# Kernel tuning notes

Hardware: AMD Instinct MI355X
Metric: run time of the kernel (lower is better)

Reference implementation:

```python
import jax, jax.numpy as jnp
import numpy as np

NUM_BINS = 16  # matches init kwarg num_bins


def setup_inputs() -> dict:
    key = jax.random.key(0)
    k1, k2, k3, k4, k5, k6, k7 = jax.random.split(key, 7)
    N, D, E, F = 100000, 256, 3200000, 4
    HID, NCLS = 256, 40
    x = jax.random.normal(k1, (N, D), dtype=jnp.float32)
    edge_index = jax.random.randint(k2, (E, 2), 0, N, dtype=jnp.int32)
    edge_features = jax.random.randint(k3, (E, F), 0, NUM_BINS, dtype=jnp.int32)
    # Dense layer params (keras Dense: y = x @ W + b)
    W1 = jax.random.normal(k4, (D, HID), dtype=jnp.float32) * 0.05
    b1 = jnp.zeros((HID,), dtype=jnp.float32)
    W2 = jax.random.normal(k5, (HID + F * NUM_BINS, NCLS), dtype=jnp.float32) * 0.05
    b2 = jnp.zeros((NCLS,), dtype=jnp.float32)
    return {"x": x, "edge_index": edge_index, "edge_features": edge_features,
            "W1": W1, "b1": b1, "W2": W2, "b2": b2}


def reference(x, edge_index, edge_features, W1, b1, W2, b2):
    N = x.shape[0]
    E, F = edge_features.shape

    h = jax.nn.relu(x @ W1 + b1)  # conv1: [N, HID]

    # per-feature one-hot + concat along axis 1 == reshape of [E,F,BINS]
    enc = jax.nn.one_hot(edge_features, NUM_BINS, dtype=h.dtype).reshape(E, F * NUM_BINS)

    seg = edge_index[:, 0]  # [E] node ids in [0, N)
    # Replicate tf.unique first-appearance indexing:
    #   segment_indices[j] = rank (by first appearance) of seg[j]
    #   mapped[e] = segment_indices[seg[e]] = rank[seg[seg[e]]]
    pos = jnp.full((N,), E, dtype=jnp.int32).at[seg].min(
        jnp.arange(E, dtype=jnp.int32))           # first edge position per node id
    rank = jnp.zeros((N,), jnp.int32).at[jnp.argsort(pos)].set(
        jnp.arange(N, dtype=jnp.int32))           # first-appearance rank per node id
    mapped = rank[jnp.take(seg, seg)]             # valid since N <= E

    # unsorted_segment_sum + zero padding to N rows == segment_sum with N segments
    agg = jax.ops.segment_sum(enc, mapped, num_segments=N)  # [N, F*BINS]

    z = jax.nn.relu(jnp.concatenate([h, agg], axis=1))
    return z @ W2 + b2  # conv2: [N, NCLS]
```

## Files before the change

### kernel.cpp

```cpp
#include <hip/hip_runtime.h>
#include <hip/hip_bf16.h>

#define WCHUNK 16
#define EPB  8192
#define TPB_MB 1024
#define BROWS 128
#define BCAP 16384

typedef __attribute__((ext_vector_type(8))) short bhalf8;
typedef __attribute__((ext_vector_type(4))) float floatx4;

__device__ __forceinline__ unsigned short f2bf(float f) {
    __hip_bfloat16 h = __float2bfloat16(f);
    union { __hip_bfloat16 h; unsigned short u; } v;
    v.h = h;
    return v.u;
}

__global__ void k_preps(const float* __restrict__ x, unsigned short* __restrict__ xbf,
                        const float* __restrict__ W1, const float* __restrict__ W2,
                        unsigned short* __restrict__ W1T, unsigned short* __restrict__ W2T,
                        int* __restrict__ pos, int* __restrict__ cursorb,
                        unsigned long long* __restrict__ bitmap,
                        int N, int total4, int nbuck, int W, int E, int nb_x, int nb_i) {
    int bid = blockIdx.x;
    int tid = threadIdx.x;
    if (bid < nb_x) {
        int f = bid * 256 + tid;
        if (f >= total4) return;
        int tile = f >> 12;
        int row = (f >> 6) & 63;
        int c4 = (f & 63) * 4;
        int grow = tile * 64 + row;
        float4 v = (grow < N) ? *reinterpret_cast<const float4*>(x + (size_t)grow * 256 + c4)
                              : make_float4(0.f, 0.f, 0.f, 0.f);
        ushort4 bv;
        bv.x = f2bf(v.x); bv.y = f2bf(v.y); bv.z = f2bf(v.z); bv.w = f2bf(v.w);
        int uidx = (row * 256 + c4) ^ ((row & 7) << 3);
        *reinterpret_cast<ushort4*>(&xbf[(size_t)tile * 16384 + uidx]) = bv;
    } else if (bid < nb_x + nb_i) {
        int i = (bid - nb_x) * 256 + tid;
        if (i < N) pos[i] = E;
        if (i < nbuck) cursorb[i] = i * BCAP;
        if (i < W) bitmap[i] = 0ull;
    } else {
        int i = (bid - nb_x - nb_i) * 256 + tid;
        if (i < 256 * 256) {
            int c = i >> 8, k = i & 255;
            W1T[i] = f2bf(W1[k * 256 + c]);
        }
        if (i < 48 * 320) {
            int c = i / 320, k = i % 320;
            W2T[i] = (c < 40) ? f2bf(W2[k * 40 + c]) : (unsigned short)0;
        }
    }
}

__global__ void k_posmin(const int* __restrict__ ei, int* __restrict__ pos, int Escan) {
    int e = blockIdx.x * blockDim.x + threadIdx.x;
    if (e < Escan) {
        int s = ((const int2*)ei)[e].x;
        if (pos[s] > e) atomicMin(&pos[s], e);
    }
}

__global__ void k_bitmap(const int* __restrict__ pos, unsigned long long* __restrict__ bitmap,
                         int N, int E) {
    int n = blockIdx.x * blockDim.x + threadIdx.x;
    if (n < N) {
        int p = pos[n];
        if (p < E) atomicOr(&bitmap[p >> 6], 1ull << (p & 63));
    }
}

__global__ void k_bitsum(const unsigned long long* __restrict__ bitmap,
                         int* __restrict__ bsum, int W) {
    __shared__ int sdata[256];
    int t = threadIdx.x;
    int base = (blockIdx.x * 256 + t) * WCHUNK;
    int cnt = 0;
    for (int l = 0; l < WCHUNK; l++) {
        int i = base + l;
        if (i < W) cnt += __popcll(bitmap[i]);
    }
    sdata[t] = cnt;
    __syncthreads();
    for (int s = 128; s > 0; s >>= 1) {
        if (t < s) sdata[t] += sdata[t + s];
        __syncthreads();
    }
    if (t == 0) bsum[blockIdx.x] = sdata[0];
}

__global__ void k_scanbsum(int* __restrict__ bsum, int nblk) {
    __shared__ int part[1024];
    const int T = 1024;
    int t = threadIdx.x;
    int per = (nblk + T - 1) / T;
    int s0 = t * per, s1 = min(s0 + per, nblk);
    int sum = 0;
    for (int i = s0; i < s1; i++) sum += bsum[i];
    part[t] = sum;
    __syncthreads();
    for (int off = 1; off < T; off <<= 1) {
        int v = 0;
        if (t >= off) v = part[t - off];
        __syncthreads();
        part[t] += v;
        __syncthreads();
    }
    int run = part[t] - sum;
    for (int i = s0; i < s1; i++) {
        int old = bsum[i];
        bsum[i] = run;
        run += old;
    }
    if (t == T - 1) bsum[nblk] = part[T - 1];
}

__global__ void k_wordpfx(const unsigned long long* __restrict__ bitmap,
                          const int* __restrict__ bsum, int* __restrict__ wordpfx, int W) {
    __shared__ int sdata[256];
    int t = threadIdx.x;
    int base = (blockIdx.x * 256 + t) * WCHUNK;
    int cnt = 0;
    for (int l = 0; l < WCHUNK; l++) {
        int i = base + l;
        if (i < W) cnt += __popcll(bitmap[i]);
    }
    sdata[t] = cnt;
    __syncthreads();
    for (int off = 1; off < 256; off <<= 1) {
        int v = 0;
        if (t >= off) v = sdata[t - off];
        __syncthreads();
        sdata[t] += v;
        __syncthreads();
    }
    int run = bsum[blockIdx.x] + sdata[t] - cnt;
    for (int l = 0; l < WCHUNK; l++) {
        int i = base + l;
        if (i >= W) break;
        wordpfx[i] = run;
        run += __popcll(bitmap[i]);
    }
}

__global__ void k_rt(const int* __restrict__ ei, const int* __restrict__ pos,
                     const unsigned long long* __restrict__ bitmap,
                     const int* __restrict__ wordpfx, int* __restrict__ rt, int N) {
    int n = blockIdx.x * blockDim.x + threadIdx.x;
    if (n >= N) return;
    int sn = ((const int2*)ei)[n].x;
    int p = pos[sn];
    int w = p >> 6, off = p & 63;
    unsigned long long mask = (1ull << off) - 1ull;
    rt[n] = wordpfx[w] + __popcll(bitmap[w] & mask);
}

__global__ __launch_bounds__(TPB_MB, 4) void k_mebin(const int* __restrict__ ei,
                                                     const int* __restrict__ rt,
                                                     const int* __restrict__ ef,
                                                     int* __restrict__ cursorb,
                                                     unsigned* __restrict__ binned,
                                                     int E, int nbuck) {
    __shared__ unsigned lmp[EPB];
    __shared__ int lcnt[800];
    __shared__ int lbase[800];
    __shared__ int lfill[800];
    int tid = threadIdx.x;
    int base = blockIdx.x * EPB;
    for (int b = tid; b < nbuck; b += TPB_MB) { lcnt[b] = 0; lfill[b] = 0; }
    __syncthreads();
#pragma unroll
    for (int jj = 0; jj < 2; jj++) {
        int l0 = (jj * 4 + 0) * TPB_MB + tid;
        int l1 = (jj * 4 + 1) * TPB_MB + tid;
        int l2 = (jj * 4 + 2) * TPB_MB + tid;
        int l3 = (jj * 4 + 3) * TPB_MB + tid;
        int e0 = base + l0, e1 = base + l1, e2 = base + l2, e3 = base + l3;
        int s0 = 0, s1 = 0, s2 = 0, s3 = 0;
        if (e0 < E) s0 = ((const int2*)ei)[e0].x;
        if (e1 < E) s1 = ((const int2*)ei)[e1].x;
        if (e2 < E) s2 = ((const int2*)ei)[e2].x;
        if (e3 < E) s3 = ((const int2*)ei)[e3].x;
        int m0 = 0, m1 = 0, m2 = 0, m3 = 0;
        if (e0 < E) m0 = rt[s0];
        if (e1 < E) m1 = rt[s1];
        if (e2 < E) m2 = rt[s2];
        if (e3 < E) m3 = rt[s3];
        int4 f0, f1, f2, f3;
        if (e0 < E) f0 = *reinterpret_cast<const int4*>(ef + 4 * (size_t)e0);
        if (e1 < E) f1 = *reinterpret_cast<const int4*>(ef + 4 * (size_t)e1);
        if (e2 < E) f2 = *reinterpret_cast<const int4*>(ef + 4 * (size_t)e2);
        if (e3 < E) f3 = *reinterpret_cast<const int4*>(ef + 4 * (size_t)e3);
        if (e0 < E) { lmp[l0] = ((unsigned)m0 << 16) | (unsigned)(f0.x | (f0.y << 4) | (f0.z << 8) | (f0.w << 12)); atomicAdd(&lcnt[m0 >> 7], 1); }
        if (e1 < E) { lmp[l1] = ((unsigned)m1 << 16) | (unsigned)(f1.x | (f1.y << 4) | (f1.z << 8) | (f1.w << 12)); atomicAdd(&lcnt[m1 >> 7], 1); }
        if (e2 < E) { lmp[l2] = ((unsigned)m2 << 16) | (unsigned)(f2.x | (f2.y << 4) | (f2.z << 8) | (f2.w << 12)); atomicAdd(&lcnt[m2 >> 7], 1); }
        if (e3 < E) { lmp[l3] = ((unsigned)m3 << 16) | (unsigned)(f3.x | (f3.y << 4) | (f3.z << 8) | (f3.w << 12)); atomicAdd(&lcnt[m3 >> 7], 1); }
    }
    __syncthreads();
    for (int b = tid; b < nbuck; b += TPB_MB) {
        int c = lcnt[b];
        lbase[b] = (c > 0) ? atomicAdd(&cursorb[b], c) : 0;
    }
    __syncthreads();
#pragma unroll
    for (int j = 0; j < EPB / TPB_MB; j++) {
        int li = j * TPB_MB + tid;
        if (base + li < E) {
            unsigned v = lmp[li];
            int b = v >> 23;
            int off = atomicAdd(&lfill[b], 1);
            long long slot = (long long)lbase[b] + off;
            if (slot < (long long)(b + 1) * BCAP)
                binned[slot] = v & 0x7FFFFFu;
        }
    }
}

__global__ __launch_bounds__(256) void k_bgather(const int* __restrict__ cursorb,
                                                 const unsigned* __restrict__ binned,
                                                 unsigned short* __restrict__ aggbf, int N) {
    __shared__ int hist[BROWS * 64];
    int tid = threadIdx.x;
    int b = blockIdx.x;
    int m0 = b * BROWS;
    for (int i = tid; i < BROWS * 64; i += 256) hist[i] = 0;
    __syncthreads();
    int r0 = b * BCAP;
    int r1 = min(cursorb[b], (b + 1) * BCAP);
    for (int i = r0 + tid; i < r1; i += 256) {
        unsigned v = binned[i];
        int lr = (int)(v >> 16) << 6;
        atomicAdd(&hist[lr + (v & 15u)], 1);
        atomicAdd(&hist[lr + 16 + ((v >> 4) & 15u)], 1);
        atomicAdd(&hist[lr + 32 + ((v >> 8) & 15u)], 1);
        atomicAdd(&hist[lr + 48 + ((v >> 12) & 15u)], 1);
    }
    __syncthreads();
    int rows = min(BROWS, N - m0);
    for (int i = tid; i < rows * 64; i += 256) {
        int lr = i >> 6, col = i & 63;
        int tile = (m0 + lr) >> 6;
        int row = (m0 + lr) & 63;
        int uidx = (row * 64 + col) ^ ((row & 7) << 3);
        aggbf[(size_t)tile * 4096 + uidx] = f2bf((float)hist[i]);
    }
}

__global__ __launch_bounds__(512) void k_fused(const unsigned short* __restrict__ xbf,
                                               const unsigned short* __restrict__ W1T,
                                               const float* __restrict__ b1,
                                               const unsigned short* __restrict__ W2T,
                                               const float* __restrict__ b2,
                                               const unsigned short* __restrict__ aggbf,
                                               float* __restrict__ out, int N) {
    __shared__ __align__(16) unsigned short xs[64 * 256];
    __shared__ __align__(16) unsigned short as[64 * 64];
    int tid = threadIdx.x;
    int lane = tid & 63;
    int w = tid >> 6;
    int lrow = lane & 15, lkb = lane >> 4;
    int n0 = blockIdx.x * 64;

    {
        const char* xg = (const char*)(xbf + (size_t)blockIdx.x * 16384);
#pragma unroll
        for (int j = 0; j < 4; j++) {
            int ch = w * 4 + j;
            __builtin_amdgcn_global_load_lds(
                (const __attribute__((address_space(1))) unsigned*)(xg + ch * 1024 + lane * 16),
                (__attribute__((address_space(3))) unsigned*)((char*)xs + ch * 1024),
                16, 0, 0);
        }
        const char* ag = (const char*)(aggbf + (size_t)blockIdx.x * 4096);
        __builtin_amdgcn_global_load_lds(
            (const __attribute__((address_space(1))) unsigned*)(ag + w * 1024 + lane * 16),
            (__attribute__((address_space(3))) unsigned*)((char*)as + w * 1024),
            16, 0, 0);
    }
    __syncthreads();

    int wc0 = w * 32;
    floatx4 acc1[4][2];
#pragma unroll
    for (int mt = 0; mt < 4; mt++)
#pragma unroll
        for (int nt = 0; nt < 2; nt++) acc1[mt][nt] = (floatx4){0.f, 0.f, 0.f, 0.f};
    float b1v[2];
#pragma unroll
    for (int nt = 0; nt < 2; nt++) b1v[nt] = b1[wc0 + nt * 16 + lrow];

#pragma unroll
    for (int ks = 0; ks < 8; ks++) {
        int koff = ks * 32 + lkb * 8;
        bhalf8 af[4], bf[2];
#pragma unroll
        for (int mt = 0; mt < 4; mt++) {
            int row = mt * 16 + lrow;
            int uidx = (row * 256 + koff) ^ ((row & 7) << 3);
            af[mt] = *reinterpret_cast<const bhalf8*>(&xs[uidx]);
        }
#pragma unroll
        for (int nt = 0; nt < 2; nt++) {
            int col = wc0 + nt * 16 + lrow;
            bf[nt] = *reinterpret_cast<const bhalf8*>(&W1T[(size_t)col * 256 + koff]);
        }
#pragma unroll
        for (int mt = 0; mt < 4; mt++)
#pragma unroll
            for (int nt = 0; nt < 2; nt++)
                acc1[mt][nt] = __builtin_amdgcn_mfma_f32_16x16x32_bf16(af[mt], bf[nt], acc1[mt][nt], 0, 0, 0);
    }
    __syncthreads();

#pragma unroll
    for (int mt = 0; mt < 4; mt++)
#pragma unroll
        for (int nt = 0; nt < 2; nt++) {
            int col = wc0 + nt * 16 + lrow;
#pragma unroll
            for (int r = 0; r < 4; r++) {
                int row = mt * 16 + lkb * 4 + r;
                float v = fmaxf(acc1[mt][nt][r] + b1v[nt], 0.f);
                int uidx = (row * 256 + col) ^ ((row & 7) << 3);
                xs[uidx] = f2bf(v);
            }
        }
    __syncthreads();

    int r0 = (w >> 1) * 16;
    int odd = w & 1;
    floatx4 acc2[2];
    acc2[0] = (floatx4){0.f, 0.f, 0.f, 0.f};
    acc2[1] = (floatx4){0.f, 0.f, 0.f, 0.f};
    int c0 = odd ? 32 : 0;
#pragma unroll
    for (int ks = 0; ks < 8; ks++) {
        int koff = ks * 32 + lkb * 8;
        int row = r0 + lrow;
        int uidx = (row * 256 + koff) ^ ((row & 7) << 3);
        bhalf8 a = *reinterpret_cast<const bhalf8*>(&xs[uidx]);
        bhalf8 b0 = *reinterpret_cast<const bhalf8*>(&W2T[(size_t)(c0 + lrow) * 320 + koff]);
        acc2[0] = __builtin_amdgcn_mfma_f32_16x16x32_bf16(a, b0, acc2[0], 0, 0, 0);
        if (!odd) {
            bhalf8 b1f = *reinterpret_cast<const bhalf8*>(&W2T[(size_t)(16 + lrow) * 320 + koff]);
            acc2[1] = __builtin_amdgcn_mfma_f32_16x16x32_bf16(a, b1f, acc2[1], 0, 0, 0);
        }
    }
#pragma unroll
    for (int ks = 0; ks < 2; ks++) {
        int koff = ks * 32 + lkb * 8;
        int row = r0 + lrow;
        int uidx = (row * 64 + koff) ^ ((row & 7) << 3);
        bhalf8 a = *reinterpret_cast<const bhalf8*>(&as[uidx]);
        bhalf8 b0 = *reinterpret_cast<const bhalf8*>(&W2T[(size_t)(c0 + lrow) * 320 + 256 + koff]);
        acc2[0] = __builtin_amdgcn_mfma_f32_16x16x32_bf16(a, b0, acc2[0], 0, 0, 0);
        if (!odd) {
            bhalf8 b1f = *reinterpret_cast<const bhalf8*>(&W2T[(size_t)(16 + lrow) * 320 + 256 + koff]);
            acc2[1] = __builtin_amdgcn_mfma_f32_16x16x32_bf16(a, b1f, acc2[1], 0, 0, 0);
        }
    }
    int ntend = odd ? 1 : 2;
#pragma unroll
    for (int nt = 0; nt < 2; nt++) {
        if (nt >= ntend) continue;
        int col = c0 + nt * 16 + lrow;
        if (col >= 40) continue;
        float bb = b2[col];
#pragma unroll
        for (int r = 0; r < 4; r++) {
            int row = n0 + r0 + lkb * 4 + r;
            if (row < N) out[(size_t)row * 40 + col] = acc2[nt][r] + bb;
        }
    }
}

extern "C" void kernel_launch(void* const* d_in, const int* in_sizes, int n_in,
                              void* d_out, int out_size, void* d_ws, size_t ws_size,
                              hipStream_t stream) {
    const float* x  = (const float*)d_in[0];
    const int*   ei = (const int*)d_in[1];
    const int*   ef = (const int*)d_in[2];
    const float* W1 = (const float*)d_in[3];
    const float* b1 = (const float*)d_in[4];
    const float* W2 = (const float*)d_in[5];
    const float* b2 = (const float*)d_in[6];
    float* out = (float*)d_out;

    const int HID = in_sizes[4];
    const int D   = in_sizes[3] / HID;
    const int N   = in_sizes[0] / D;
    const int E   = in_sizes[1] / 2;
    (void)HID; (void)D;

    const int Escan  = min(N, E);
    const int nbuck  = (N + BROWS - 1) / BROWS;
    const int ntiles = (N + 63) / 64;
    const int W      = (Escan + 63) / 64;
    const int nblk_w = (W + 4096 - 1) / 4096;

    int* ws = (int*)d_ws;
    size_t o = 0;
    unsigned short* aggbf = (unsigned short*)(ws + o); o += (size_t)ntiles * 2048;
    int* pos = ws + o;                               o += N;
    int* rt = ws + o;                                o += N;
    int* cursorb = ws + o;                           o += nbuck;
    int* bsum_w = ws + o;                            o += nblk_w + 1;
    o = (o + 1) & ~(size_t)1;
    unsigned long long* bitmap = (unsigned long long*)(ws + o); o += 2 * (size_t)W;
    int* wordpfx = ws + o;                           o += W + 1;
    o = (o + 3) & ~(size_t)3;
    unsigned* binned = (unsigned*)(ws + o);          o += (size_t)nbuck * BCAP;
    unsigned short* W1T = (unsigned short*)(ws + o); o += 32768;
    unsigned short* W2T = (unsigned short*)(ws + o); o += 7680;
    unsigned short* xbf = (unsigned short*)(ws + o); o += (size_t)ntiles * 8192;

    const int total4 = ntiles * 4096;
    const int nb_x = (total4 + 255) / 256;
    const int nb_i = (max(max(N, W), nbuck) + 255) / 256;
    const int nb_w = 256;

    hipLaunchKernelGGL(k_preps, dim3(nb_x + nb_i + nb_w), dim3(256), 0, stream,
                       x, xbf, W1, W2, W1T, W2T, pos, cursorb, bitmap,
                       N, total4, nbuck, W, E, nb_x, nb_i);
    hipLaunchKernelGGL(k_posmin, dim3((Escan + 255) / 256), dim3(256), 0, stream, ei, pos, Escan);
    hipLaunchKernelGGL(k_bitmap, dim3((N + 255) / 256), dim3(256), 0, stream, pos, bitmap, N, E);
    hipLaunchKernelGGL(k_bitsum, dim3(nblk_w), dim3(256), 0, stream, bitmap, bsum_w, W);
    hipLaunchKernelGGL(k_scanbsum, dim3(1), dim3(1024), 0, stream, bsum_w, nblk_w);
    hipLaunchKernelGGL(k_wordpfx, dim3(nblk_w), dim3(256), 0, stream, bitmap, bsum_w, wordpfx, W);
    hipLaunchKernelGGL(k_rt, dim3((N + 255) / 256), dim3(256), 0, stream, ei, pos, bitmap, wordpfx, rt, N);
    hipLaunchKernelGGL(k_mebin, dim3((E + EPB - 1) / EPB), dim3(TPB_MB), 0, stream,
                       ei, rt, ef, cursorb, binned, E, nbuck);
    hipLaunchKernelGGL(k_bgather, dim3(nbuck), dim3(256), 0, stream, cursorb, binned, aggbf, N);
    hipLaunchKernelGGL(k_fused, dim3(ntiles), dim3(512), 0, stream,
                       xbf, W1T, b1, W2T, b2, aggbf, out, N);
}
```

Before: 187.5 us.

## Replace three-kernel bitmap scan with single-block scan and double x-conversion work per block

Merges the block-sum, block-scan and word-prefix kernels into one single-block 1024-thread kernel that popcounts the bitmap words and writes the word prefix directly, removing two kernel launches and the intermediate block-sum buffer. With roughly 1563 bitmap words this is about two words per thread, so one block is sufficient. The x-to-bf16 conversion in the prep kernel now handles two float4 elements per thread, halving the number of blocks it launches. The single-block scan would serialize badly if W grew large.

```diff
diff --git a/kernel.cpp b/kernel.cpp
--- a/kernel.cpp
+++ b/kernel.cpp
@@ -1,7 +1,6 @@
 #include <hip/hip_runtime.h>
 #include <hip/hip_bf16.h>
 
-#define WCHUNK 16
 #define EPB  8192
 #define TPB_MB 1024
 #define BROWS 128
@@ -26,18 +25,21 @@
     int bid = blockIdx.x;
     int tid = threadIdx.x;
     if (bid < nb_x) {
-        int f = bid * 256 + tid;
-        if (f >= total4) return;
-        int tile = f >> 12;
-        int row = (f >> 6) & 63;
-        int c4 = (f & 63) * 4;
-        int grow = tile * 64 + row;
-        float4 v = (grow < N) ? *reinterpret_cast<const float4*>(x + (size_t)grow * 256 + c4)
-                              : make_float4(0.f, 0.f, 0.f, 0.f);
-        ushort4 bv;
-        bv.x = f2bf(v.x); bv.y = f2bf(v.y); bv.z = f2bf(v.z); bv.w = f2bf(v.w);
-        int uidx = (row * 256 + c4) ^ ((row & 7) << 3);
-        *reinterpret_cast<ushort4*>(&xbf[(size_t)tile * 16384 + uidx]) = bv;
+#pragma unroll
+        for (int j = 0; j < 2; j++) {
+            int f = bid * 512 + j * 256 + tid;
+            if (f >= total4) continue;
+            int tile = f >> 12;
+            int row = (f >> 6) & 63;
+            int c4 = (f & 63) * 4;
+            int grow = tile * 64 + row;
+            float4 v = (grow < N) ? *reinterpret_cast<const float4*>(x + (size_t)grow * 256 + c4)
+                                  : make_float4(0.f, 0.f, 0.f, 0.f);
+            ushort4 bv;
+            bv.x = f2bf(v.x); bv.y = f2bf(v.y); bv.z = f2bf(v.z); bv.w = f2bf(v.w);
+            int uidx = (row * 256 + c4) ^ ((row & 7) << 3);
+            *reinterpret_cast<ushort4*>(&xbf[(size_t)tile * 16384 + uidx]) = bv;
+        }
     } else if (bid < nb_x + nb_i) {
         int i = (bid - nb_x) * 256 + tid;
         if (i < N) pos[i] = E;
@@ -73,33 +75,15 @@
     }
 }
 
-__global__ void k_bitsum(const unsigned long long* __restrict__ bitmap,
-                         int* __restrict__ bsum, int W) {
-    __shared__ int sdata[256];
-    int t = threadIdx.x;
-    int base = (blockIdx.x * 256 + t) * WCHUNK;
-    int cnt = 0;
-    for (int l = 0; l < WCHUNK; l++) {
-        int i = base + l;
-        if (i < W) cnt += __popcll(bitmap[i]);
-    }
-    sdata[t] = cnt;
-    __syncthreads();
-    for (int s = 128; s > 0; s >>= 1) {
-        if (t < s) sdata[t] += sdata[t + s];
-        __syncthreads();
-    }
-    if (t == 0) bsum[blockIdx.x] = sdata[0];
-}
-
-__global__ void k_scanbsum(int* __restrict__ bsum, int nblk) {
+__global__ void k_scanw(const unsigned long long* __restrict__ bitmap,
+                        int* __restrict__ wordpfx, int W) {
     __shared__ int part[1024];
     const int T = 1024;
     int t = threadIdx.x;
-    int per = (nblk + T - 1) / T;
-    int s0 = t * per, s1 = min(s0 + per, nblk);
+    int per = (W + T - 1) / T;
+    int s0 = t * per, s1 = min(s0 + per, W);
     int sum = 0;
-    for (int i = s0; i < s1; i++) sum += bsum[i];
+    for (int i = s0; i < s1; i++) sum += __popcll(bitmap[i]);
     part[t] = sum;
     __syncthreads();
     for (int off = 1; off < T; off <<= 1) {
@@ -111,39 +95,10 @@
     }
     int run = part[t] - sum;
     for (int i = s0; i < s1; i++) {
-        int old = bsum[i];
-        bsum[i] = run;
-        run += old;
-    }
-    if (t == T - 1) bsum[nblk] = part[T - 1];
-}
-
-__global__ void k_wordpfx(const unsigned long long* __restrict__ bitmap,
-                          const int* __restrict__ bsum, int* __restrict__ wordpfx, int W) {
-    __shared__ int sdata[256];
-    int t = threadIdx.x;
-    int base = (blockIdx.x * 256 + t) * WCHUNK;
-    int cnt = 0;
-    for (int l = 0; l < WCHUNK; l++) {
-        int i = base + l;
-        if (i < W) cnt += __popcll(bitmap[i]);
-    }
-    sdata[t] = cnt;
-    __syncthreads();
-    for (int off = 1; off < 256; off <<= 1) {
-        int v = 0;
-        if (t >= off) v = sdata[t - off];
-        __syncthreads();
-        sdata[t] += v;
-        __syncthreads();
-    }
-    int run = bsum[blockIdx.x] + sdata[t] - cnt;
-    for (int l = 0; l < WCHUNK; l++) {
-        int i = base + l;
-        if (i >= W) break;
         wordpfx[i] = run;
         run += __popcll(bitmap[i]);
     }
+    if (t == T - 1) wordpfx[W] = part[T - 1];
 }
 
 __global__ void k_rt(const int* __restrict__ ei, const int* __restrict__ pos,
@@ -399,7 +354,6 @@
     const int nbuck  = (N + BROWS - 1) / BROWS;
     const int ntiles = (N + 63) / 64;
     const int W      = (Escan + 63) / 64;
-    const int nblk_w = (W + 4096 - 1) / 4096;
 
     int* ws = (int*)d_ws;
     size_t o = 0;
@@ -407,7 +361,6 @@
     int* pos = ws + o;                               o += N;
     int* rt = ws + o;                                o += N;
     int* cursorb = ws + o;                           o += nbuck;
-    int* bsum_w = ws + o;                            o += nblk_w + 1;
     o = (o + 1) & ~(size_t)1;
     unsigned long long* bitmap = (unsigned long long*)(ws + o); o += 2 * (size_t)W;
     int* wordpfx = ws + o;                           o += W + 1;
@@ -418,7 +371,7 @@
     unsigned short* xbf = (unsigned short*)(ws + o); o += (size_t)ntiles * 8192;
 
     const int total4 = ntiles * 4096;
-    const int nb_x = (total4 + 255) / 256;
+    const int nb_x = (total4 + 511) / 512;
     const int nb_i = (max(max(N, W), nbuck) + 255) / 256;
     const int nb_w = 256;
 
@@ -427,9 +380,7 @@
                        N, total4, nbuck, W, E, nb_x, nb_i);
     hipLaunchKernelGGL(k_posmin, dim3((Escan + 255) / 256), dim3(256), 0, stream, ei, pos, Escan);
     hipLaunchKernelGGL(k_bitmap, dim3((N + 255) / 256), dim3(256), 0, stream, pos, bitmap, N, E);
-    hipLaunchKernelGGL(k_bitsum, dim3(nblk_w), dim3(256), 0, stream, bitmap, bsum_w, W);
-    hipLaunchKernelGGL(k_scanbsum, dim3(1), dim3(1024), 0, stream, bsum_w, nblk_w);
-    hipLaunchKernelGGL(k_wordpfx, dim3(nblk_w), dim3(256), 0, stream, bitmap, bsum_w, wordpfx, W);
+    hipLaunchKernelGGL(k_scanw, dim3(1), dim3(1024), 0, stream, bitmap, wordpfx, W);
     hipLaunchKernelGGL(k_rt, dim3((N + 255) / 256), dim3(256), 0, stream, ei, pos, bitmap, wordpfx, rt, N);
     hipLaunchKernelGGL(k_mebin, dim3((E + EPB - 1) / EPB), dim3(TPB_MB), 0, stream,
                        ei, rt, ef, cursorb, binned, E, nbuck);
```

Result: faster. 176.9 us (-5.6%).
